# Performance work log

Hardware: AMD Instinct MI355X
Metric: run time of the kernel (lower is better)

The kernel has to match this reference:

```python
import jax, jax.numpy as jnp
import numpy as np

B, T, C, U = 256, 512, 256, 64  # batch, time, classes (incl. blank), label length
BLANK = C - 1                   # keras ctc_batch_cost: blank is last class
S = 2 * U + 1                   # extended label length (blanks interleaved)
NEG = -1e30                     # safe log-zero for fp32
EPS = 1e-7                      # keras.backend.epsilon()


def setup_inputs() -> dict:
    key = jax.random.key(0)
    k1, k2 = jax.random.split(key)
    # y_pred are softmax probabilities over time, as fed to ctc_batch_cost
    y_pred = jax.nn.softmax(jax.random.normal(k1, (B, T, C), dtype=jnp.float32), axis=-1)
    # labels exclude the blank index (values in [0, C-2]); all U positions valid
    y_true = jax.random.randint(k2, (B, U), 0, C - 1, dtype=jnp.int32)
    return {"y_true": y_true, "y_pred": y_pred}


def _ctc_loss(y_pred, y_true):
    # keras ctc_batch_cost computes loss on log(y_pred + eps)
    log_probs = jnp.log(y_pred + EPS)                      # [B, T, C]
    # extended label sequence: blank, l1, blank, l2, ..., blank
    ext = jnp.full((B, S), BLANK, dtype=y_true.dtype).at[:, 1::2].set(y_true)
    # gather per-state emission log-probs: lp_ext[b,t,s] = log_probs[b,t,ext[b,s]]
    lp_ext = jnp.take_along_axis(log_probs, ext[:, None, :].astype(jnp.int32), axis=2)  # [B,T,S]
    # skip transition (s-2 -> s) allowed iff ext[s] != blank and ext[s] != ext[s-2]
    ext_m2 = jnp.pad(ext[:, :-2], ((0, 0), (2, 0)), constant_values=-1)
    skip_ok = (ext != BLANK) & (ext != ext_m2)             # [B, S]

    # alpha_0: can start in state 0 (blank) or state 1 (first label)
    alpha0 = (jnp.full((B, S), NEG, dtype=jnp.float32)
              .at[:, 0].set(lp_ext[:, 0, 0])
              .at[:, 1].set(lp_ext[:, 0, 1]))

    def step(alpha, lp_t):
        a1 = jnp.pad(alpha[:, :-1], ((0, 0), (1, 0)), constant_values=NEG)
        a2 = jnp.pad(alpha[:, :-2], ((0, 0), (2, 0)), constant_values=NEG)
        a2 = jnp.where(skip_ok, a2, NEG)
        alpha = jnp.logaddexp(jnp.logaddexp(alpha, a1), a2) + lp_t
        return alpha, None

    lp_time_major = jnp.swapaxes(lp_ext, 0, 1)             # [T, B, S]
    alpha, _ = jax.lax.scan(step, alpha0, lp_time_major[1:])
    # terminate in last blank or last label
    loss = -jnp.logaddexp(alpha[:, -1], alpha[:, -2])      # [B]
    return loss[:, None]                                   # [B, 1] like ctc_batch_cost


def reference(y_true, y_pred):
    return _ctc_loss(y_pred, y_true)
```

## Files before the change

kernel.cpp:

```cpp
#include <hip/hip_runtime.h>


constexpr int B = 256, T = 512, C = 256, U = 64;
constexpr int CH = 16;
#define EPSF 1e-7f

__device__ __forceinline__ float dpp_wave_shr1(float x) {
    return __int_as_float(__builtin_amdgcn_update_dpp(
        0, __float_as_int(x), 0x138, 0xf, 0xf, true));
}

#define LOAD_CHUNK(LA, BL, cidx)                                          \
    {                                                                     \
        const int c_ = (cidx);                                            \
        _Pragma("unroll")                                                 \
        for (int i = 0; i < CH; ++i) {                                    \
            int t = 1 + c_ * CH + i;                                      \
            t = t < T ? t : T - 1;                                        \
            LA[i] = labp[(size_t)t * C];                                  \
            BL[i] = blkp[(size_t)t * C];                                  \
        }                                                                 \
    }

#define DPPMAX(ctrl)                                                      \
    {                                                                     \
        float x_ = __int_as_float(__builtin_amdgcn_update_dpp(            \
            0, __float_as_int(m_), (ctrl), 0xf, 0xf, true));              \
        m_ = fmaxf(m_, x_);                                               \
    }

#define RESCALE()                                                         \
    {                                                                     \
        float m_ = fmaxf(fmaxf(a_even, a_odd), a_top);                    \
        DPPMAX(0x111) DPPMAX(0x112) DPPMAX(0x114) DPPMAX(0x118)           \
        DPPMAX(0x142) DPPMAX(0x143)                                       \
        const float mx_ = __int_as_float(                                 \
            __builtin_amdgcn_readlane(__float_as_int(m_), 63));           \
        int e_ = (__float_as_int(mx_) >> 23) & 0xff;                      \
        int k_ = 187 - e_;                                                \
        k_ = k_ > 127 ? 127 : k_;                                         \
        const float s_ = __int_as_float((k_ + 127) << 23);                \
        a_even *= s_; a_odd *= s_; a_top *= s_;                           \
        esum += k_;                                                       \
    }

#define COMP_CHUNK(LA, BL, cidx)                                          \
    {                                                                     \
        const int c_ = (cidx);                                            \
        _Pragma("unroll")                                                 \
        for (int i = 0; i < CH; ++i) {                                    \
            const int t = 1 + c_ * CH + i;                                \
            if (t < T) {                                                  \
                const float pb = BL[i] + EPSF;                            \
                const float pl = LA[i] + EPSF;                            \
                const float po = dpp_wave_shr1(a_odd);                    \
                const float skp = skip_ok ? po : 0.f;                     \
                const float ne = (a_even + po) * pb;                      \
                const float no = (a_odd + a_even + skp) * pl;             \
                const float nt = (a_top + a_odd) * pb;                    \
                a_even = ne; a_odd = no; a_top = nt;                      \
                if ((t & 7) == 0) RESCALE();                              \
            }                                                             \
        }                                                                 \
    }

__global__ __launch_bounds__(64) void ctc_kernel(const int* __restrict__ y_true,
                                                 const float* __restrict__ y_pred,
                                                 float* __restrict__ out) {
    const int b = blockIdx.x;
    const int lane = threadIdx.x;
    const int label = y_true[b * U + lane];
    const int label_prev = __shfl_up(label, 1);
    const bool skip_ok = (lane > 0) && (label != label_prev);
    const float* __restrict__ rowp = y_pred + (size_t)b * (T * C);
    const float* __restrict__ labp = rowp + label;
    const float* __restrict__ blkp = rowp + (C - 1);

    float a_even, a_odd, a_top;
    {
        const float pb = blkp[0] + EPSF;
        const float pl = labp[0] + EPSF;
        a_even = (lane == 0) ? pb : 0.f;
        a_odd  = (lane == 0) ? pl : 0.f;
        a_top  = 0.f;
    }
    int esum = 0;

    float la0[CH], bl0[CH], la1[CH], bl1[CH];
    LOAD_CHUNK(la0, bl0, 0);

    for (int c2 = 0; c2 < 16; ++c2) {
        const int c = 2 * c2;
        LOAD_CHUNK(la1, bl1, c + 1);
        __builtin_amdgcn_sched_barrier(0);
        COMP_CHUNK(la0, bl0, c);
        if (c2 < 15) LOAD_CHUNK(la0, bl0, c + 2);
        __builtin_amdgcn_sched_barrier(0);
        COMP_CHUNK(la1, bl1, c + 1);
    }

    if (lane == 63)
        out[b] = -logf(a_top + a_odd) + (float)esum * 0.69314718055994531f;
}

extern "C" void kernel_launch(void* const* d_in, const int* in_sizes, int n_in,
                              void* d_out, int out_size, void* d_ws, size_t ws_size,
                              hipStream_t stream) {
    const int* y_true   = (const int*)d_in[0];
    const float* y_pred = (const float*)d_in[1];
    float* out = (float*)d_out;
    hipLaunchKernelGGL(ctc_kernel, dim3(B), dim3(64), 0, stream,
                       y_true, y_pred, out);
}
```

Measured before the change: 202.1 us.

## Warp-specialize CTC kernel: producer waves stream rows into LDS ring buffer

Splits each block into one compute wave and three producer waves. The producers copy full 16-timestep chunks of y_pred rows into a triple-buffered LDS ring using coalesced float4 loads. The compute wave reads label and blank probabilities from LDS with a four-step register prefetch, replacing the strided per-lane global gathers that sat on the recurrence's critical path. The cost is a block-wide barrier per chunk, reading the whole row instead of only the needed columns, and 48KB of LDS per block, which limits occupancy. The initial step is now folded into the loop and the rescale timing is shifted.

```diff
diff --git a/kernel.cpp b/kernel.cpp
--- a/kernel.cpp
+++ b/kernel.cpp
@@ -2,25 +2,13 @@
 
 
 constexpr int B = 256, T = 512, C = 256, U = 64;
-constexpr int CH = 16;
+constexpr int CH = 16, NCH = T / CH;
 #define EPSF 1e-7f
 
 __device__ __forceinline__ float dpp_wave_shr1(float x) {
     return __int_as_float(__builtin_amdgcn_update_dpp(
         0, __float_as_int(x), 0x138, 0xf, 0xf, true));
 }
-
-#define LOAD_CHUNK(LA, BL, cidx)                                          \
-    {                                                                     \
-        const int c_ = (cidx);                                            \
-        _Pragma("unroll")                                                 \
-        for (int i = 0; i < CH; ++i) {                                    \
-            int t = 1 + c_ * CH + i;                                      \
-            t = t < T ? t : T - 1;                                        \
-            LA[i] = labp[(size_t)t * C];                                  \
-            BL[i] = blkp[(size_t)t * C];                                  \
-        }                                                                 \
-    }
 
 #define DPPMAX(ctrl)                                                      \
     {                                                                     \
@@ -44,63 +32,94 @@
         esum += k_;                                                       \
     }
 
-#define COMP_CHUNK(LA, BL, cidx)                                          \
-    {                                                                     \
-        const int c_ = (cidx);                                            \
-        _Pragma("unroll")                                                 \
-        for (int i = 0; i < CH; ++i) {                                    \
-            const int t = 1 + c_ * CH + i;                                \
-            if (t < T) {                                                  \
-                const float pb = BL[i] + EPSF;                            \
-                const float pl = LA[i] + EPSF;                            \
-                const float po = dpp_wave_shr1(a_odd);                    \
-                const float skp = skip_ok ? po : 0.f;                     \
-                const float ne = (a_even + po) * pb;                      \
-                const float no = (a_odd + a_even + skp) * pl;             \
-                const float nt = (a_top + a_odd) * pb;                    \
-                a_even = ne; a_odd = no; a_top = nt;                      \
-                if ((t & 7) == 0) RESCALE();                              \
-            }                                                             \
-        }                                                                 \
+__global__ __launch_bounds__(256, 1) void ctc_kernel(const int* __restrict__ y_true,
+                                                     const float* __restrict__ y_pred,
+                                                     float* __restrict__ out) {
+    __shared__ float lds[3 * CH * C];
+    const int b = blockIdx.x;
+    const int lane = threadIdx.x & 63;
+    const int wid = threadIdx.x >> 6;
+    const float* __restrict__ rowp = y_pred + (size_t)b * T * C;
+
+    if (wid) {
+        const int pw = wid - 1;
+#pragma unroll 1
+        for (int c = 0; c < 2; ++c) {
+            float4 g[6];
+#pragma unroll
+            for (int n = 0; n < 6; ++n) {
+                const int j = pw + 3 * n;
+                if (j < CH) g[n] = ((const float4*)(rowp + (size_t)(c * CH + j) * C))[lane];
+            }
+#pragma unroll
+            for (int n = 0; n < 6; ++n) {
+                const int j = pw + 3 * n;
+                if (j < CH) ((float4*)&lds[(c * CH + j) * C])[lane] = g[n];
+            }
+        }
+        __syncthreads();
+        int ws = 2;
+#pragma unroll 1
+        for (int k = 0; k < NCH; ++k) {
+            const int c = k + 2;
+            if (c < NCH) {
+                float4 g[6];
+#pragma unroll
+                for (int n = 0; n < 6; ++n) {
+                    const int j = pw + 3 * n;
+                    if (j < CH) g[n] = ((const float4*)(rowp + (size_t)(c * CH + j) * C))[lane];
+                }
+#pragma unroll
+                for (int n = 0; n < 6; ++n) {
+                    const int j = pw + 3 * n;
+                    if (j < CH) ((float4*)&lds[(ws * CH + j) * C])[lane] = g[n];
+                }
+            }
+            __syncthreads();
+            ws = ws + 1; if (ws == 3) ws = 0;
+        }
+    } else {
+        const int label = y_true[b * U + lane];
+        const int label_prev = __shfl_up(label, 1);
+        const bool skip_ok = (lane > 0) && (label != label_prev);
+        __syncthreads();
+
+        float plab[4], pblk[4];
+#pragma unroll
+        for (int t = 0; t < 4; ++t) {
+            plab[t] = lds[t * C + label];
+            pblk[t] = lds[t * C + (C - 1)];
+        }
+        float a_even = (lane == 0) ? 1.f : 0.f, a_odd = 0.f, a_top = 0.f;
+        int esum = 0, cs = 0;
+#pragma unroll 1
+        for (int k = 0; k < NCH; ++k) {
+            int ns = cs + 1; if (ns == 3) ns = 0;
+#pragma unroll
+            for (int i = 0; i < CH; ++i) {
+                const int t = k * CH + i;
+                const float pb = pblk[i & 3] + EPSF;
+                const float pl = plab[i & 3] + EPSF;
+                {
+                    int srow = (i < 12) ? (cs * CH + i + 4) : (ns * CH + (i - 12));
+                    if (t + 4 >= T) srow = cs * CH + 15;
+                    plab[i & 3] = lds[srow * C + label];
+                    pblk[i & 3] = lds[srow * C + (C - 1)];
+                }
+                const float po = dpp_wave_shr1(a_odd);
+                const float skp = skip_ok ? po : 0.f;
+                const float ne = (a_even + po) * pb;
+                const float no = (a_even + a_odd + skp) * pl;
+                const float nt = (a_top + a_odd) * pb;
+                a_even = ne; a_odd = no; a_top = nt;
+                if ((t & 7) == 7) RESCALE();
+            }
+            __syncthreads();
+            cs = ns;
+        }
+        if (lane == 63)
+            out[b] = -logf(a_top + a_odd) + (float)esum * 0.69314718055994531f;
     }
-
-__global__ __launch_bounds__(64) void ctc_kernel(const int* __restrict__ y_true,
-                                                 const float* __restrict__ y_pred,
-                                                 float* __restrict__ out) {
-    const int b = blockIdx.x;
-    const int lane = threadIdx.x;
-    const int label = y_true[b * U + lane];
-    const int label_prev = __shfl_up(label, 1);
-    const bool skip_ok = (lane > 0) && (label != label_prev);
-    const float* __restrict__ rowp = y_pred + (size_t)b * (T * C);
-    const float* __restrict__ labp = rowp + label;
-    const float* __restrict__ blkp = rowp + (C - 1);
-
-    float a_even, a_odd, a_top;
-    {
-        const float pb = blkp[0] + EPSF;
-        const float pl = labp[0] + EPSF;
-        a_even = (lane == 0) ? pb : 0.f;
-        a_odd  = (lane == 0) ? pl : 0.f;
-        a_top  = 0.f;
-    }
-    int esum = 0;
-
-    float la0[CH], bl0[CH], la1[CH], bl1[CH];
-    LOAD_CHUNK(la0, bl0, 0);
-
-    for (int c2 = 0; c2 < 16; ++c2) {
-        const int c = 2 * c2;
-        LOAD_CHUNK(la1, bl1, c + 1);
-        __builtin_amdgcn_sched_barrier(0);
-        COMP_CHUNK(la0, bl0, c);
-        if (c2 < 15) LOAD_CHUNK(la0, bl0, c + 2);
-        __builtin_amdgcn_sched_barrier(0);
-        COMP_CHUNK(la1, bl1, c + 1);
-    }
-
-    if (lane == 63)
-        out[b] = -logf(a_top + a_odd) + (float)esum * 0.69314718055994531f;
 }
 
 extern "C" void kernel_launch(void* const* d_in, const int* in_sizes, int n_in,
@@ -109,6 +128,6 @@
     const int* y_true   = (const int*)d_in[0];
     const float* y_pred = (const float*)d_in[1];
     float* out = (float*)d_out;
-    hipLaunchKernelGGL(ctc_kernel, dim3(B), dim3(64), 0, stream,
+    hipLaunchKernelGGL(ctc_kernel, dim3(B), dim3(256), 0, stream,
                        y_true, y_pred, out);
 }
```

Result: slower. 283.4 us (+40.3%).

## Split CTC into parallel gather pass and compact serial recurrence

Applied to the files above, without the earlier changes.

Adds a highly parallel gather kernel that streams y_pred with coalesced float4 loads and writes the label and blank probabilities into a compact [B,T,68] workspace. The serial alpha recurrence then reads this compact array instead of scattered 4-byte loads strided by C. It also folds the t=0 step into the loop by starting from a unit initial state. The cost is a second launch plus an extra write and read of the compact buffer, and the old path is used only when the workspace is too small.

```diff
diff --git a/kernel.cpp b/kernel.cpp
--- a/kernel.cpp
+++ b/kernel.cpp
@@ -3,24 +3,13 @@
 
 constexpr int B = 256, T = 512, C = 256, U = 64;
 constexpr int CH = 16;
+constexpr int STR = 68;
 #define EPSF 1e-7f
 
 __device__ __forceinline__ float dpp_wave_shr1(float x) {
     return __int_as_float(__builtin_amdgcn_update_dpp(
         0, __float_as_int(x), 0x138, 0xf, 0xf, true));
 }
-
-#define LOAD_CHUNK(LA, BL, cidx)                                          \
-    {                                                                     \
-        const int c_ = (cidx);                                            \
-        _Pragma("unroll")                                                 \
-        for (int i = 0; i < CH; ++i) {                                    \
-            int t = 1 + c_ * CH + i;                                      \
-            t = t < T ? t : T - 1;                                        \
-            LA[i] = labp[(size_t)t * C];                                  \
-            BL[i] = blkp[(size_t)t * C];                                  \
-        }                                                                 \
-    }
 
 #define DPPMAX(ctrl)                                                      \
     {                                                                     \
@@ -44,57 +33,89 @@
         esum += k_;                                                       \
     }
 
+#define LOAD_CHUNK(LA, BL, cidx, LP, BP, STRIDE)                          \
+    {                                                                     \
+        const int c_ = (cidx);                                            \
+        _Pragma("unroll")                                                 \
+        for (int i = 0; i < CH; ++i) {                                    \
+            int t = c_ * CH + i;                                          \
+            t = t < T ? t : T - 1;                                        \
+            LA[i] = LP[(size_t)t * STRIDE];                               \
+            BL[i] = BP[(size_t)t * STRIDE];                               \
+        }                                                                 \
+    }
+
 #define COMP_CHUNK(LA, BL, cidx)                                          \
     {                                                                     \
         const int c_ = (cidx);                                            \
         _Pragma("unroll")                                                 \
         for (int i = 0; i < CH; ++i) {                                    \
-            const int t = 1 + c_ * CH + i;                                \
-            if (t < T) {                                                  \
-                const float pb = BL[i] + EPSF;                            \
-                const float pl = LA[i] + EPSF;                            \
-                const float po = dpp_wave_shr1(a_odd);                    \
-                const float skp = skip_ok ? po : 0.f;                     \
-                const float ne = (a_even + po) * pb;                      \
-                const float no = (a_odd + a_even + skp) * pl;             \
-                const float nt = (a_top + a_odd) * pb;                    \
-                a_even = ne; a_odd = no; a_top = nt;                      \
-                if ((t & 7) == 0) RESCALE();                              \
-            }                                                             \
+            const int t = c_ * CH + i;                                    \
+            const float pb = BL[i] + EPSF;                                \
+            const float pl = LA[i] + EPSF;                                \
+            const float po = dpp_wave_shr1(a_odd);                        \
+            const float skp = skip_ok ? po : 0.f;                         \
+            const float ne = (a_even + po) * pb;                          \
+            const float no = (a_even + a_odd + skp) * pl;                 \
+            const float nt = (a_top + a_odd) * pb;                        \
+            a_even = ne; a_odd = no; a_top = nt;                          \
+            if ((t & 7) == 7) RESCALE();                                  \
         }                                                                 \
     }
 
-__global__ __launch_bounds__(64) void ctc_kernel(const int* __restrict__ y_true,
-                                                 const float* __restrict__ y_pred,
-                                                 float* __restrict__ out) {
+__global__ __launch_bounds__(256) void gather_kernel(const int* __restrict__ y_true,
+                                                     const float* __restrict__ y_pred,
+                                                     float* __restrict__ compact) {
+    __shared__ float buf[4][2][C];
+    const int lane = threadIdx.x & 63;
+    const int w = threadIdx.x >> 6;
+    const int g = blockIdx.x;
+    const int b = g >> 3;
+    const int r0 = (g & 7) * 64 + w;
+    const int lab = y_true[b * U + lane];
+    const float* __restrict__ rp = y_pred + (size_t)b * T * C;
+    float* __restrict__ cp = compact + (size_t)b * T * STR;
+
+    float4 v = ((const float4*)(rp + (size_t)r0 * C))[lane];
+#pragma unroll
+    for (int i = 0; i < 16; ++i) {
+        const int r = r0 + 4 * i;
+        float4 vn = v;
+        if (i < 15) vn = ((const float4*)(rp + (size_t)(r + 4) * C))[lane];
+        float* bb = &buf[w][i & 1][0];
+        ((float4*)bb)[lane] = v;
+        const float sel = bb[lab];
+        cp[(size_t)r * STR + lane] = sel;
+        if (lane == 0) cp[(size_t)r * STR + 64] = bb[C - 1];
+        v = vn;
+    }
+}
+
+template <int STRIDE, bool COMPACT>
+__global__ __launch_bounds__(64) void chain_kernel(const int* __restrict__ y_true,
+                                                   const float* __restrict__ src,
+                                                   float* __restrict__ out) {
     const int b = blockIdx.x;
     const int lane = threadIdx.x;
     const int label = y_true[b * U + lane];
     const int label_prev = __shfl_up(label, 1);
     const bool skip_ok = (lane > 0) && (label != label_prev);
-    const float* __restrict__ rowp = y_pred + (size_t)b * (T * C);
-    const float* __restrict__ labp = rowp + label;
-    const float* __restrict__ blkp = rowp + (C - 1);
+    const float* __restrict__ base = src + (size_t)b * T * STRIDE;
+    const float* __restrict__ labp = COMPACT ? (base + lane) : (base + label);
+    const float* __restrict__ blkp = COMPACT ? (base + 64) : (base + (C - 1));
 
-    float a_even, a_odd, a_top;
-    {
-        const float pb = blkp[0] + EPSF;
-        const float pl = labp[0] + EPSF;
-        a_even = (lane == 0) ? pb : 0.f;
-        a_odd  = (lane == 0) ? pl : 0.f;
-        a_top  = 0.f;
-    }
+    float a_even = (lane == 0) ? 1.f : 0.f, a_odd = 0.f, a_top = 0.f;
     int esum = 0;
 
     float la0[CH], bl0[CH], la1[CH], bl1[CH];
-    LOAD_CHUNK(la0, bl0, 0);
+    LOAD_CHUNK(la0, bl0, 0, labp, blkp, STRIDE);
 
     for (int c2 = 0; c2 < 16; ++c2) {
         const int c = 2 * c2;
-        LOAD_CHUNK(la1, bl1, c + 1);
+        LOAD_CHUNK(la1, bl1, c + 1, labp, blkp, STRIDE);
         __builtin_amdgcn_sched_barrier(0);
         COMP_CHUNK(la0, bl0, c);
-        if (c2 < 15) LOAD_CHUNK(la0, bl0, c + 2);
+        if (c2 < 15) LOAD_CHUNK(la0, bl0, c + 2, labp, blkp, STRIDE);
         __builtin_amdgcn_sched_barrier(0);
         COMP_CHUNK(la1, bl1, c + 1);
     }
@@ -109,6 +130,15 @@
     const int* y_true   = (const int*)d_in[0];
     const float* y_pred = (const float*)d_in[1];
     float* out = (float*)d_out;
-    hipLaunchKernelGGL(ctc_kernel, dim3(B), dim3(64), 0, stream,
-                       y_true, y_pred, out);
+    const size_t need = (size_t)B * T * STR * sizeof(float);
+    if (ws_size >= need) {
+        float* compact = (float*)d_ws;
+        hipLaunchKernelGGL(gather_kernel, dim3(2048), dim3(256), 0, stream,
+                           y_true, y_pred, compact);
+        hipLaunchKernelGGL((chain_kernel<STR, true>), dim3(B), dim3(64), 0, stream,
+                           y_true, compact, out);
+    } else {
+        hipLaunchKernelGGL((chain_kernel<C, false>), dim3(B), dim3(64), 0, stream,
+                           y_true, y_pred, out);
+    }
 }
```

New measurement: 225.7 us. +11.7%, slower.

## Stream full rows via coalesced float4 loads and gather emissions from LDS

Applied to the files above, without the earlier changes.

Replaces per-lane strided scalar loads of label and blank probabilities with coalesced float4 loads of whole 8-timestep row blocks, double-buffered in registers. Rows are staged through an 8-slot LDS ring so each lane then gathers its label and blank values from shared memory. This targets the uncoalesced, sector-wasting global gathers on the serial recurrence path. The cost is reading all 256 classes per timestep instead of two, plus LDS traffic and extra register pressure. The initial step is folded into the loop by starting from alpha=1 at lane 0.

```diff
diff --git a/kernel.cpp b/kernel.cpp
--- a/kernel.cpp
+++ b/kernel.cpp
@@ -2,25 +2,12 @@
 
 
 constexpr int B = 256, T = 512, C = 256, U = 64;
-constexpr int CH = 16;
 #define EPSF 1e-7f
 
 __device__ __forceinline__ float dpp_wave_shr1(float x) {
     return __int_as_float(__builtin_amdgcn_update_dpp(
         0, __float_as_int(x), 0x138, 0xf, 0xf, true));
 }
-
-#define LOAD_CHUNK(LA, BL, cidx)                                          \
-    {                                                                     \
-        const int c_ = (cidx);                                            \
-        _Pragma("unroll")                                                 \
-        for (int i = 0; i < CH; ++i) {                                    \
-            int t = 1 + c_ * CH + i;                                      \
-            t = t < T ? t : T - 1;                                        \
-            LA[i] = labp[(size_t)t * C];                                  \
-            BL[i] = blkp[(size_t)t * C];                                  \
-        }                                                                 \
-    }
 
 #define DPPMAX(ctrl)                                                      \
     {                                                                     \
@@ -44,59 +31,70 @@
         esum += k_;                                                       \
     }
 
-#define COMP_CHUNK(LA, BL, cidx)                                          \
+#define CHUNK(CUR, NXT, kexpr)                                            \
     {                                                                     \
-        const int c_ = (cidx);                                            \
+        const int k_ = (kexpr);                                           \
+        if (k_ < 63) {                                                    \
+            const float4* np_ = rp4 + (size_t)(k_ + 1) * 512;             \
+            _Pragma("unroll")                                             \
+            for (int j = 0; j < 8; ++j) NXT[j] = np_[j * 64];             \
+        }                                                                 \
+        __builtin_amdgcn_sched_barrier(0);                                \
         _Pragma("unroll")                                                 \
-        for (int i = 0; i < CH; ++i) {                                    \
-            const int t = 1 + c_ * CH + i;                                \
-            if (t < T) {                                                  \
-                const float pb = BL[i] + EPSF;                            \
-                const float pl = LA[i] + EPSF;                            \
-                const float po = dpp_wave_shr1(a_odd);                    \
-                const float skp = skip_ok ? po : 0.f;                     \
-                const float ne = (a_even + po) * pb;                      \
-                const float no = (a_odd + a_even + skp) * pl;             \
-                const float nt = (a_top + a_odd) * pb;                    \
-                a_even = ne; a_odd = no; a_top = nt;                      \
-                if ((t & 7) == 0) RESCALE();                              \
+        for (int i = 0; i < 8; ++i) {                                     \
+            const float pb = pblk[i & 3] + EPSF;               \
+            const float pl = plab[i & 3] + EPSF;                          \
+            if (i < 3) {                               \
+                ((float4*)&lds[((i + 5) & 7) * C])[lane] = CUR[i + 5];    \
+            } else if (k_ < 63) {                                         \
+                ((float4*)&lds[((i + 5) & 7) * C])[lane] = NXT[i - 3];    \
             }                                                             \
+            if (i < 4 || k_ < 63) {                   \
+                plab[i & 3] = lds[((i + 4) & 7) * C + label];             \
+                pblk[i & 3] = lds[((i + 4) & 7) * C + (C - 1)];           \
+            }                                                             \
+            const float po = dpp_wave_shr1(a_odd);       \
+            const float skp = skip_ok ? po : 0.f;                         \
+            const float ne = (a_even + po) * pb;                          \
+            const float no = (a_even + a_odd + skp) * pl;                 \
+            const float nt = (a_top + a_odd) * pb;                        \
+            a_even = ne; a_odd = no; a_top = nt;                          \
+            if (i == 7) RESCALE();                                        \
         }                                                                 \
     }
 
 __global__ __launch_bounds__(64) void ctc_kernel(const int* __restrict__ y_true,
                                                  const float* __restrict__ y_pred,
                                                  float* __restrict__ out) {
+    __shared__ float lds[8 * C];
     const int b = blockIdx.x;
     const int lane = threadIdx.x;
     const int label = y_true[b * U + lane];
     const int label_prev = __shfl_up(label, 1);
     const bool skip_ok = (lane > 0) && (label != label_prev);
-    const float* __restrict__ rowp = y_pred + (size_t)b * (T * C);
-    const float* __restrict__ labp = rowp + label;
-    const float* __restrict__ blkp = rowp + (C - 1);
+    const float4* __restrict__ rp4 =
+        (const float4*)(y_pred + (size_t)b * T * C) + lane;
 
-    float a_even, a_odd, a_top;
-    {
-        const float pb = blkp[0] + EPSF;
-        const float pl = labp[0] + EPSF;
-        a_even = (lane == 0) ? pb : 0.f;
-        a_odd  = (lane == 0) ? pl : 0.f;
-        a_top  = 0.f;
+    float4 bufA[8], bufB[8];
+#pragma unroll
+    for (int j = 0; j < 8; ++j) bufA[j] = rp4[j * 64];
+#pragma unroll
+    for (int j = 0; j < 5; ++j)
+        ((float4*)&lds[j * C])[lane] = bufA[j];
+    float plab[4], pblk[4];
+#pragma unroll
+    for (int j = 0; j < 4; ++j) {
+        plab[j] = lds[j * C + label];
+        pblk[j] = lds[j * C + (C - 1)];
     }
+
+    float a_even = (lane == 0) ? 1.f : 0.f, a_odd = 0.f, a_top = 0.f;
     int esum = 0;
 
-    float la0[CH], bl0[CH], la1[CH], bl1[CH];
-    LOAD_CHUNK(la0, bl0, 0);
-
-    for (int c2 = 0; c2 < 16; ++c2) {
-        const int c = 2 * c2;
-        LOAD_CHUNK(la1, bl1, c + 1);
-        __builtin_amdgcn_sched_barrier(0);
-        COMP_CHUNK(la0, bl0, c);
-        if (c2 < 15) LOAD_CHUNK(la0, bl0, c + 2);
-        __builtin_amdgcn_sched_barrier(0);
-        COMP_CHUNK(la1, bl1, c + 1);
+#pragma unroll 1
+    for (int kk = 0; kk < 64; kk += 2) {
+        CHUNK(bufA, bufB, kk);
+        CHUNK(bufB, bufA, kk + 1);
     }
 
     if (lane == 63)
```

Result: slower. 248.3 us (+22.9%).
